# Optimization experiments

Hardware: AMD Instinct MI355X
Metric: run time of the kernel (lower is better)

## Reference

```python
import jax, jax.numpy as jnp
import numpy as np

HIDDEN = 1024
NUM_HEADS = 16
HEAD_DIM = HIDDEN // NUM_HEADS
EPS = 1e-05


def setup_inputs() -> dict:
    key = jax.random.key(0)
    ks = jax.random.split(key, 6)
    B, S = 4, 2048
    x = jax.random.normal(ks[0], (B, S, HIDDEN), dtype=jnp.float32)
    # trunc_normal_(std=0.02) approximated by scaled normal
    w_in = jax.random.normal(ks[1], (3 * HIDDEN, HIDDEN), dtype=jnp.float32) * 0.02
    b_in = jax.random.normal(ks[2], (3 * HIDDEN,), dtype=jnp.float32) * 0.02
    w_norm = jnp.ones((HIDDEN,), dtype=jnp.float32)
    lim = 1.0 / np.sqrt(HIDDEN)
    w_out = jax.random.uniform(ks[3], (HIDDEN, HIDDEN), dtype=jnp.float32, minval=-lim, maxval=lim)
    b_out = jax.random.uniform(ks[4], (HIDDEN,), dtype=jnp.float32, minval=-lim, maxval=lim)
    return {"x": x, "w_in": w_in, "b_in": b_in, "w_norm": w_norm, "w_out": w_out, "b_out": b_out}


def _rms_norm(x, w, eps):
    var = jnp.mean(jnp.square(x), axis=-1, keepdims=True)
    return x * jax.lax.rsqrt(var + eps) * w


def reference(x, w_in, b_in, w_norm, w_out, b_out):
    B, S, _ = x.shape
    xn = _rms_norm(x, w_norm, EPS)
    qkv = jnp.einsum('bsd,ed->bse', xn, w_in) + b_in  # [B,S,3*HIDDEN]
    q, k, v = jnp.split(qkv, 3, axis=-1)
    # [B,S,H*D] -> [B,H,S,D]
    def split_heads(t):
        return t.reshape(B, S, NUM_HEADS, HEAD_DIM).transpose(0, 2, 1, 3)
    q, k, v = split_heads(q), split_heads(k), split_heads(v)
    scale = 1.0 / np.sqrt(HEAD_DIM)
    scores = jnp.einsum('bhqd,bhkd->bhqk', q, k) * scale
    attn = jax.nn.softmax(scores, axis=-1)
    o = jnp.einsum('bhqk,bhkd->bhqd', attn, v)
    o = o.transpose(0, 2, 1, 3).reshape(B, S, HIDDEN)
    return jnp.einsum('bsd,ed->bse', o, w_out) + b_out
```

## Files before the change

### kernel.cpp

```cpp
#include <hip/hip_runtime.h>
#include <stdint.h>

typedef short bf16x4 __attribute__((ext_vector_type(4)));
typedef short bf16x8 __attribute__((ext_vector_type(8)));
typedef _Float16 f16x8 __attribute__((ext_vector_type(8)));
typedef float f32x4 __attribute__((ext_vector_type(4)));
typedef float f32x16 __attribute__((ext_vector_type(16)));
typedef unsigned int u32x4 __attribute__((ext_vector_type(4)));
typedef unsigned int u32x2 __attribute__((ext_vector_type(2)));

#if __has_builtin(__builtin_amdgcn_exp2f)
#define EXP2 __builtin_amdgcn_exp2f
#else
#define EXP2 exp2f
#endif

__device__ __forceinline__ short f2bf(float f) {
  union { float f; uint32_t u; } v; v.f = f;
  uint32_t r = (v.u + 0x7fffu + ((v.u >> 16) & 1u)) >> 16;
  return (short)(uint16_t)r;
}

__device__ __forceinline__ unsigned cvtpk_bf16(float lo, float hi) {
  unsigned r;
  asm("v_cvt_pk_bf16_f32 %0, %1, %2" : "=v"(r) : "v"(lo), "v"(hi));
  return r;
}

#if __has_builtin(__builtin_amdgcn_permlane32_swap)
__device__ __forceinline__ void plane32_swap(unsigned& a, unsigned& b) {
  u32x2 r = __builtin_amdgcn_permlane32_swap(a, b, false, false);
  a = r[0]; b = r[1];
}
__device__ __forceinline__ float xhalf_max(float x) {
  unsigned xu = __builtin_bit_cast(unsigned, x);
  u32x2 r = __builtin_amdgcn_permlane32_swap(xu, xu, false, false);
  return fmaxf(__builtin_bit_cast(float, r[0]), __builtin_bit_cast(float, r[1]));
}
__device__ __forceinline__ float xhalf_sum(float x) {
  unsigned xu = __builtin_bit_cast(unsigned, x);
  u32x2 r = __builtin_amdgcn_permlane32_swap(xu, xu, false, false);
  return __builtin_bit_cast(float, r[0]) + __builtin_bit_cast(float, r[1]);
}
#else
__device__ __forceinline__ void plane32_swap(unsigned& a, unsigned& b) {
  asm("s_nop 1\n\tv_permlane32_swap_b32 %0, %1" : "+v"(a), "+v"(b));
}
__device__ __forceinline__ float xhalf_max(float x) { return fmaxf(x, __shfl_xor(x, 32, 64)); }
__device__ __forceinline__ float xhalf_sum(float x) { return x + __shfl_xor(x, 32, 64); }
#endif

__device__ __forceinline__ float fmax3(float a, float b, float c) {
  return fmaxf(fmaxf(a, b), c);
}

__device__ __forceinline__ float tmax16(const f32x16& s) {
  float a0 = fmax3(s[0], s[1], s[2]);
  float a1 = fmax3(s[3], s[4], s[5]);
  float a2 = fmax3(s[6], s[7], s[8]);
  float a3 = fmax3(s[9], s[10], s[11]);
  float a4 = fmax3(s[12], s[13], s[14]);
  float b0 = fmax3(a0, a1, s[15]);
  float b1 = fmax3(a2, a3, a4);
  return fmaxf(b0, b1);
}
__device__ __forceinline__ float tsum16(const f32x16& s) {
  float a0 = (s[0] + s[1]) + (s[2] + s[3]);
  float a1 = (s[4] + s[5]) + (s[6] + s[7]);
  float a2 = (s[8] + s[9]) + (s[10] + s[11]);
  float a3 = (s[12] + s[13]) + (s[14] + s[15]);
  return (a0 + a1) + (a2 + a3);
}

__device__ __forceinline__ f32x16 zero16() {
  f32x16 z;
#pragma unroll
  for (int i = 0; i < 16; ++i) z[i] = 0.f;
  return z;
}

__device__ __forceinline__ void gld_lds16(const void* g, void* l) {
  __builtin_amdgcn_global_load_lds(
      (__attribute__((address_space(1))) const void*)g,
      (__attribute__((address_space(3))) void*)l, 16, 0, 0);
}

__global__ __launch_bounds__(256) void k_rmsnorm(const float* __restrict__ x,
                                                 const float* __restrict__ wn,
                                                 short* __restrict__ xn) {
  const int row = blockIdx.x;
  const int t = threadIdx.x;
  const float4 v = reinterpret_cast<const float4*>(x + (size_t)row * 1024)[t];
  float ss = v.x * v.x + v.y * v.y + v.z * v.z + v.w * v.w;
#pragma unroll
  for (int m = 32; m >= 1; m >>= 1) ss += __shfl_xor(ss, m, 64);
  __shared__ float red[4];
  if ((t & 63) == 0) red[t >> 6] = ss;
  __syncthreads();
  const float tot = red[0] + red[1] + red[2] + red[3];
  const float rr = rsqrtf(tot * (1.0f / 1024.0f) + 1e-5f);
  const float4 g = reinterpret_cast<const float4*>(wn)[t];
  bf16x4 o;
  o[0] = f2bf(v.x * rr * g.x);
  o[1] = f2bf(v.y * rr * g.y);
  o[2] = f2bf(v.z * rr * g.z);
  o[3] = f2bf(v.w * rr * g.w);
  reinterpret_cast<bf16x4*>(xn + (size_t)row * 1024)[t] = o;
}

__global__ __launch_bounds__(256) void k_cast_bf(const float* __restrict__ in,
                                                 short* __restrict__ out, int n4) {
  int i = blockIdx.x * 256 + threadIdx.x;
  if (i >= n4) return;
  float4 v = reinterpret_cast<const float4*>(in)[i];
  bf16x4 o;
  o[0] = f2bf(v.x); o[1] = f2bf(v.y); o[2] = f2bf(v.z); o[3] = f2bf(v.w);
  reinterpret_cast<bf16x4*>(out)[i] = o;
}

__global__ __launch_bounds__(256) void k_cast_f16(const float* __restrict__ in,
                                                  _Float16* __restrict__ out, int n4) {
  int i = blockIdx.x * 256 + threadIdx.x;
  if (i >= n4) return;
  float4 v = reinterpret_cast<const float4*>(in)[i];
  _Float16 o[4] = {(_Float16)v.x, (_Float16)v.y, (_Float16)v.z, (_Float16)v.w};
  reinterpret_cast<ulong1*>(out)[i] = *reinterpret_cast<ulong1*>(o);
}

__global__ __launch_bounds__(256) void k_gemm_qkv(const short* __restrict__ A,
                                                  const short* __restrict__ B,
                                                  const float* __restrict__ bias,
                                                  short* __restrict__ qb,
                                                  short* __restrict__ kb,
                                                  short* __restrict__ vb) {
  __shared__ __align__(16) short As[128 * 32];
  __shared__ __align__(16) short Bs[128 * 32];
  const int t = threadIdx.x;
  const int orig = blockIdx.y * 24 + blockIdx.x;
  const int swz = (orig & 7) * 192 + (orig >> 3);
  const long bn0 = (long)(swz % 24) * 128;
  const long bm0 = (long)(swz / 24) * 128;
  const int w = t >> 6, l = t & 63;
  const int wr = (w >> 1) * 64, wc = (w & 1) * 64;
  const int lm = l & 15, h = l >> 4;
  f32x4 acc[4][4];
#pragma unroll
  for (int i = 0; i < 4; ++i)
#pragma unroll
    for (int j = 0; j < 4; ++j) acc[i][j] = (f32x4){0.f, 0.f, 0.f, 0.f};
  const int srow = t >> 2, scol = (t & 3) * 8;
  const short* Ag = A + (bm0 + srow) * 1024 + scol;
  const short* Bg = B + (bn0 + srow) * 1024 + scol;
  short* AsP = As + t * 8;
  short* BsP = Bs + t * 8;
  for (int kt = 0; kt < 32; ++kt) {
    const int k0 = kt << 5;
    gld_lds16(Ag + k0, AsP);
    gld_lds16(Ag + k0 + 64 * 1024, AsP + 2048);
    gld_lds16(Bg + k0, BsP);
    gld_lds16(Bg + k0 + 64 * 1024, BsP + 2048);
    __syncthreads();
    bf16x8 af[4], bfr[4];
#pragma unroll
    for (int mi = 0; mi < 4; ++mi)
      af[mi] = *reinterpret_cast<const bf16x8*>(As + (wr + mi * 16 + lm) * 32 + h * 8);
#pragma unroll
    for (int ni = 0; ni < 4; ++ni)
      bfr[ni] = *reinterpret_cast<const bf16x8*>(Bs + (wc + ni * 16 + lm) * 32 + h * 8);
    __builtin_amdgcn_s_setprio(1);
#pragma unroll
    for (int mi = 0; mi < 4; ++mi)
#pragma unroll
      for (int ni = 0; ni < 4; ++ni)
        acc[mi][ni] = __builtin_amdgcn_mfma_f32_16x16x32_bf16(af[mi], bfr[ni], acc[mi][ni], 0, 0, 0);
    __builtin_amdgcn_s_setprio(0);
    __syncthreads();
  }
#pragma unroll
  for (int ni = 0; ni < 4; ++ni) {
    const int ncol = (int)bn0 + wc + ni * 16 + lm;
    const float bv = bias[ncol];
    const int which = ncol >> 10;
    const int e = ncol & 1023;
#pragma unroll
    for (int mi = 0; mi < 4; ++mi) {
#pragma unroll
      for (int r = 0; r < 4; ++r) {
        const long mrow = bm0 + wr + mi * 16 + h * 4 + r;
        const float val = acc[mi][ni][r] + bv;
        const long off = (((mrow >> 11) * 16 + (e >> 6)) * 2048 + (mrow & 2047)) * 64 + (e & 63);
        if (which == 0) qb[off] = f2bf(val * 0.18033688011112042f);
        else if (which == 1) kb[off] = f2bf(val);
        else vb[off] = f2bf(val);
      }
    }
  }
}

__global__ __launch_bounds__(256) void k_gemm_out(const _Float16* __restrict__ A,
                                                  const _Float16* __restrict__ B,
                                                  const float* __restrict__ bias,
                                                  float* __restrict__ outp) {
  __shared__ __align__(16) _Float16 As[128 * 32];
  __shared__ __align__(16) _Float16 Bs[128 * 32];
  const int t = threadIdx.x;
  const int orig = blockIdx.y * 8 + blockIdx.x;
  const int swz = (orig & 7) * 64 + (orig >> 3);
  const long bn0 = (long)(swz % 8) * 128;
  const long bm0 = (long)(swz / 8) * 128;
  const int w = t >> 6, l = t & 63;
  const int wr = (w >> 1) * 64, wc = (w & 1) * 64;
  const int lm = l & 15, h = l >> 4;
  f32x4 acc[4][4];
#pragma unroll
  for (int i = 0; i < 4; ++i)
#pragma unroll
    for (int j = 0; j < 4; ++j) acc[i][j] = (f32x4){0.f, 0.f, 0.f, 0.f};
  const int srow = t >> 2, scol = (t & 3) * 8;
  const _Float16* Ag = A + (bm0 + srow) * 1024 + scol;
  const _Float16* Bg = B + (bn0 + srow) * 1024 + scol;
  _Float16* AsP = As + t * 8;
  _Float16* BsP = Bs + t * 8;
  for (int kt = 0; kt < 32; ++kt) {
    const int k0 = kt << 5;
    gld_lds16(Ag + k0, AsP);
    gld_lds16(Ag + k0 + 64 * 1024, AsP + 2048);
    gld_lds16(Bg + k0, BsP);
    gld_lds16(Bg + k0 + 64 * 1024, BsP + 2048);
    __syncthreads();
    f16x8 af[4], bfr[4];
#pragma unroll
    for (int mi = 0; mi < 4; ++mi)
      af[mi] = *reinterpret_cast<const f16x8*>(As + (wr + mi * 16 + lm) * 32 + h * 8);
#pragma unroll
    for (int ni = 0; ni < 4; ++ni)
      bfr[ni] = *reinterpret_cast<const f16x8*>(Bs + (wc + ni * 16 + lm) * 32 + h * 8);
    __builtin_amdgcn_s_setprio(1);
#pragma unroll
    for (int mi = 0; mi < 4; ++mi)
#pragma unroll
      for (int ni = 0; ni < 4; ++ni)
        acc[mi][ni] = __builtin_amdgcn_mfma_f32_16x16x32_f16(af[mi], bfr[ni], acc[mi][ni], 0, 0, 0);
    __builtin_amdgcn_s_setprio(0);
    __syncthreads();
  }
#pragma unroll
  for (int ni = 0; ni < 4; ++ni) {
    const int ncol = (int)bn0 + wc + ni * 16 + lm;
    const float bv = bias[ncol];
#pragma unroll
    for (int mi = 0; mi < 4; ++mi) {
#pragma unroll
      for (int r = 0; r < 4; ++r) {
        const long mrow = bm0 + wr + mi * 16 + h * 4 + r;
        outp[mrow * 1024 + ncol] = acc[mi][ni][r] + bv;
      }
    }
  }
}

__global__ __launch_bounds__(256) void k_transpose_v(const short* __restrict__ v,
                                                     short* __restrict__ vt) {
  __shared__ short tile[64][72];
  const int bh = blockIdx.y, st = blockIdx.x;
  const int t = threadIdx.x;
  const int r = t >> 2, c0 = (t & 3) * 16;
  const short* src = v + ((size_t)(bh * 2048 + st * 64 + r)) * 64 + c0;
  bf16x8 a = *reinterpret_cast<const bf16x8*>(src);
  bf16x8 b = *reinterpret_cast<const bf16x8*>(src + 8);
#pragma unroll
  for (int j = 0; j < 8; ++j) tile[r][c0 + j] = a[j];
#pragma unroll
  for (int j = 0; j < 8; ++j) tile[r][c0 + 8 + j] = b[j];
  __syncthreads();
  __align__(16) short tmp[16];
#pragma unroll
  for (int j = 0; j < 16; ++j) tmp[j] = tile[c0 + j][r];
  short* dst = vt + ((size_t)(bh * 64 + r)) * 2048 + st * 64 + c0;
  *reinterpret_cast<bf16x8*>(dst) = *reinterpret_cast<const bf16x8*>(tmp);
  *reinterpret_cast<bf16x8*>(dst + 8) = *reinterpret_cast<const bf16x8*>(tmp + 8);
}

__global__ __launch_bounds__(256, 2) void k_attn(const short* __restrict__ q,
                                                 const short* __restrict__ k,
                                                 const short* __restrict__ vt,
                                                 _Float16* __restrict__ o) {
  __shared__ __align__(16) short Ks[4][2048];
  __shared__ __align__(16) short Vs[4][2048];
  const int orig = blockIdx.y * 8 + blockIdx.x;
  const int work = (orig & 7) * 64 + (orig >> 3);
  const int bh = work >> 3;
  const int qt = work & 7;
  const int t = threadIdx.x;
  const int w = t >> 6, l = t & 63;
  const int lq = l & 31, hh = l >> 5;
  const int xr = lq & 7;
  const int qbase = qt * 256 + w * 64;

  bf16x8 qf[2][4];
#pragma unroll
  for (int qh = 0; qh < 2; ++qh) {
    const short* qp = q + ((size_t)(bh * 2048 + qbase + qh * 32 + lq)) * 64 + hh * 8;
#pragma unroll
    for (int db = 0; db < 4; ++db)
      qf[qh][db] = *reinterpret_cast<const bf16x8*>(qp + db * 16);
  }

  const int gg = t;
  const int uK = gg ^ ((gg >> 3) & 7);
  const int vrow = gg >> 2;
  const int vcol = (gg & 3) ^ (vrow & 3);
  const short* kh = k + (size_t)bh * 2048 * 64;
  const short* vh = vt + (size_t)bh * 64 * 2048;
  const short* ksrc = kh + uK * 8;
  const short* vsrc = vh + vrow * 2048 + vcol * 8;

  int koff[4], voff[2][2];
#pragma unroll
  for (int db = 0; db < 4; ++db)
    koff[db] = (lq * 8 + ((db * 2 + hh) ^ xr)) * 8;
#pragma unroll
  for (int dt = 0; dt < 2; ++dt)
#pragma unroll
    for (int kg = 0; kg < 2; ++kg)
      voff[dt][kg] = ((dt * 32 + lq) * 4 + ((kg * 2 + hh) ^ (lq & 3))) * 8;

  f32x16 oa00 = zero16(), oa01 = zero16();
  f32x16 oa10 = zero16(), oa11 = zero16();
  float mr0 = -1e30f, mr1 = -1e30f, lr0 = 0.f, lr1 = 0.f;

#pragma unroll
  for (int p = 0; p < 3; ++p) {
    gld_lds16(ksrc + p * 2048, &Ks[p][gg * 8]);
    gld_lds16(vsrc + p * 32, &Vs[p][gg * 8]);
  }

  for (int kt = 0; kt < 64; ++kt) {
    asm volatile("s_waitcnt vmcnt(4)" ::: "memory");
    __builtin_amdgcn_s_barrier();
    int kn = kt + 3; if (kn > 63) kn = 63;
    gld_lds16(ksrc + kn * 2048, &Ks[(kt + 3) & 3][gg * 8]);
    gld_lds16(vsrc + kn * 32, &Vs[(kt + 3) & 3][gg * 8]);

    const short* kb_ = Ks[kt & 3];
    const short* vb_ = Vs[kt & 3];
    f32x16 s0 = zero16(), s1 = zero16();
    __builtin_amdgcn_s_setprio(1);
#pragma unroll
    for (int db = 0; db < 4; ++db) {
      bf16x8 kf = *reinterpret_cast<const bf16x8*>(kb_ + koff[db]);
      s0 = __builtin_amdgcn_mfma_f32_32x32x16_bf16(kf, qf[0][db], s0, 0, 0, 0);
      s1 = __builtin_amdgcn_mfma_f32_32x32x16_bf16(kf, qf[1][db], s1, 0, 0, 0);
    }
    __builtin_amdgcn_s_setprio(0);
    float tm0 = xhalf_max(tmax16(s0));
    float tm1 = xhalf_max(tmax16(s1));
    if (!__all((tm0 <= mr0 + 8.f) && (tm1 <= mr1 + 8.f))) {
      const float mn0 = fmaxf(mr0, tm0), mn1 = fmaxf(mr1, tm1);
      const float c0 = EXP2(mr0 - mn0), c1 = EXP2(mr1 - mn1);
      lr0 *= c0; lr1 *= c1;
#pragma unroll
      for (int r = 0; r < 16; ++r) {
        oa00[r] *= c0; oa01[r] *= c0;
        oa10[r] *= c1; oa11[r] *= c1;
      }
      mr0 = mn0; mr1 = mn1;
    }
#pragma unroll
    for (int r = 0; r < 16; ++r) {
      s0[r] = EXP2(s0[r] - mr0);
      s1[r] = EXP2(s1[r] - mr1);
    }
    lr0 += tsum16(s0);
    lr1 += tsum16(s1);
    __builtin_amdgcn_s_setprio(1);
#pragma unroll
    for (int kg = 0; kg < 2; ++kg) {
      const int b0 = kg * 8;
      unsigned p00 = cvtpk_bf16(s0[b0 + 0], s0[b0 + 1]);
      unsigned p01 = cvtpk_bf16(s0[b0 + 2], s0[b0 + 3]);
      unsigned p02 = cvtpk_bf16(s0[b0 + 4], s0[b0 + 5]);
      unsigned p03 = cvtpk_bf16(s0[b0 + 6], s0[b0 + 7]);
      plane32_swap(p00, p02);
      plane32_swap(p01, p03);
      u32x4 pw0 = {p00, p01, p02, p03};
      bf16x8 pf0 = *reinterpret_cast<bf16x8*>(&pw0);
      unsigned p10 = cvtpk_bf16(s1[b0 + 0], s1[b0 + 1]);
      unsigned p11 = cvtpk_bf16(s1[b0 + 2], s1[b0 + 3]);
      unsigned p12 = cvtpk_bf16(s1[b0 + 4], s1[b0 + 5]);
      unsigned p13 = cvtpk_bf16(s1[b0 + 6], s1[b0 + 7]);
      plane32_swap(p10, p12);
      plane32_swap(p11, p13);
      u32x4 pw1 = {p10, p11, p12, p13};
      bf16x8 pf1 = *reinterpret_cast<bf16x8*>(&pw1);
      bf16x8 vf0 = *reinterpret_cast<const bf16x8*>(vb_ + voff[0][kg]);
      oa00 = __builtin_amdgcn_mfma_f32_32x32x16_bf16(vf0, pf0, oa00, 0, 0, 0);
      oa10 = __builtin_amdgcn_mfma_f32_32x32x16_bf16(vf0, pf1, oa10, 0, 0, 0);
      bf16x8 vf1 = *reinterpret_cast<const bf16x8*>(vb_ + voff[1][kg]);
      oa01 = __builtin_amdgcn_mfma_f32_32x32x16_bf16(vf1, pf0, oa01, 0, 0, 0);
      oa11 = __builtin_amdgcn_mfma_f32_32x32x16_bf16(vf1, pf1, oa11, 0, 0, 0);
    }
    __builtin_amdgcn_s_setprio(0);
  }
  const float inv0 = 1.0f / xhalf_sum(lr0);
  const float inv1 = 1.0f / xhalf_sum(lr1);
  const int b = bh >> 4, hd = bh & 15;
  _Float16* ob0 = o + ((size_t)(b * 2048 + qbase + lq)) * 1024 + hd * 64;
  _Float16* ob1 = ob0 + 32 * 1024;
#pragma unroll
  for (int r2 = 0; r2 < 16; ++r2) {
    const int d0 = (r2 & 3) + 8 * (r2 >> 2) + 4 * hh;
    ob0[d0] = (_Float16)(oa00[r2] * inv0);
    ob0[d0 + 32] = (_Float16)(oa01[r2] * inv0);
    ob1[d0] = (_Float16)(oa10[r2] * inv1);
    ob1[d0 + 32] = (_Float16)(oa11[r2] * inv1);
  }
}

extern "C" void kernel_launch(void* const* d_in, const int* in_sizes, int n_in,
                              void* d_out, int out_size, void* d_ws, size_t ws_size,
                              hipStream_t stream) {
  const float* x = (const float*)d_in[0];
  const float* w_in = (const float*)d_in[1];
  const float* b_in = (const float*)d_in[2];
  const float* w_norm = (const float*)d_in[3];
  const float* w_out = (const float*)d_in[4];
  const float* b_out = (const float*)d_in[5];
  float* out = (float*)d_out;
  char* ws = (char*)d_ws;
  short* xn = (short*)(ws);
  short* win_b = (short*)(ws + 16777216);
  _Float16* wout_h = (_Float16*)(ws + 23068672);
  short* qb = (short*)(ws + 25165824);
  short* kb = (short*)(ws + 41943040);
  short* vb = (short*)(ws + 58720256);
  short* vt = (short*)(ws + 75497472);
  _Float16* ob = (_Float16*)vb;

  k_cast_bf<<<3072, 256, 0, stream>>>(w_in, win_b, 786432);
  k_cast_f16<<<1024, 256, 0, stream>>>(w_out, wout_h, 262144);
  k_rmsnorm<<<8192, 256, 0, stream>>>(x, w_norm, xn);
  k_gemm_qkv<<<dim3(24, 64), 256, 0, stream>>>(xn, win_b, b_in, qb, kb, vb);
  k_transpose_v<<<dim3(32, 64), 256, 0, stream>>>(vb, vt);
  k_attn<<<dim3(8, 64), 256, 0, stream>>>(qb, kb, vt, ob);
  k_gemm_out<<<dim3(8, 64), 256, 0, stream>>>(ob, wout_h, b_out, out);
}
```

Measured before the change: 227.4 us.

## Give each wave private K/V LDS buffers to remove block barriers

Each of the four waves now loads its own full copy of the K and V tiles into a private LDS region, double-buffered. This removes the per-iteration block-wide barrier. All K/V fragments are read into registers up front, and the next tile's global-to-LDS loads are issued right after those reads complete. The cost is four times the global/L2 traffic for K/V and a larger LDS footprint (64KB per block), plus a prefetch depth cut from 3 stages to 2.

```diff
diff --git a/kernel.cpp b/kernel.cpp
--- a/kernel.cpp
+++ b/kernel.cpp
@@ -285,8 +285,7 @@
                                                  const short* __restrict__ k,
                                                  const short* __restrict__ vt,
                                                  _Float16* __restrict__ o) {
-  __shared__ __align__(16) short Ks[4][2048];
-  __shared__ __align__(16) short Vs[4][2048];
+  __shared__ __align__(16) short lds[4][8192];
   const int orig = blockIdx.y * 8 + blockIdx.x;
   const int work = (orig & 7) * 64 + (orig >> 3);
   const int bh = work >> 3;
@@ -296,6 +295,8 @@
   const int lq = l & 31, hh = l >> 5;
   const int xr = lq & 7;
   const int qbase = qt * 256 + w * 64;
+  short* Kb = &lds[w][0];
+  short* Vb = &lds[w][4096];
 
   bf16x8 qf[2][4];
 #pragma unroll
@@ -306,14 +307,19 @@
       qf[qh][db] = *reinterpret_cast<const bf16x8*>(qp + db * 16);
   }
 
-  const int gg = t;
-  const int uK = gg ^ ((gg >> 3) & 7);
-  const int vrow = gg >> 2;
-  const int vcol = (gg & 3) ^ (vrow & 3);
   const short* kh = k + (size_t)bh * 2048 * 64;
   const short* vh = vt + (size_t)bh * 64 * 2048;
-  const short* ksrc = kh + uK * 8;
-  const short* vsrc = vh + vrow * 2048 + vcol * 8;
+  const short* ks4[4];
+  const short* vs4[4];
+#pragma unroll
+  for (int i = 0; i < 4; ++i) {
+    const int g = i * 64 + l;
+    const int uK = g ^ ((g >> 3) & 7);
+    ks4[i] = kh + uK * 8;
+    const int vr = g >> 2;
+    const int vc = (g & 3) ^ (vr & 3);
+    vs4[i] = vh + vr * 2048 + vc * 8;
+  }
 
   int koff[4], voff[2][2];
 #pragma unroll
@@ -330,27 +336,46 @@
   float mr0 = -1e30f, mr1 = -1e30f, lr0 = 0.f, lr1 = 0.f;
 
 #pragma unroll
-  for (int p = 0; p < 3; ++p) {
-    gld_lds16(ksrc + p * 2048, &Ks[p][gg * 8]);
-    gld_lds16(vsrc + p * 32, &Vs[p][gg * 8]);
-  }
-
+  for (int p = 0; p < 2; ++p) {
+#pragma unroll
+    for (int i = 0; i < 4; ++i)
+      gld_lds16(ks4[i] + p * 2048, Kb + p * 2048 + i * 512 + l * 8);
+#pragma unroll
+    for (int i = 0; i < 4; ++i)
+      gld_lds16(vs4[i] + p * 32, Vb + p * 2048 + i * 512 + l * 8);
+  }
+
+#pragma unroll 2
   for (int kt = 0; kt < 64; ++kt) {
-    asm volatile("s_waitcnt vmcnt(4)" ::: "memory");
-    __builtin_amdgcn_s_barrier();
-    int kn = kt + 3; if (kn > 63) kn = 63;
-    gld_lds16(ksrc + kn * 2048, &Ks[(kt + 3) & 3][gg * 8]);
-    gld_lds16(vsrc + kn * 32, &Vs[(kt + 3) & 3][gg * 8]);
-
-    const short* kb_ = Ks[kt & 3];
-    const short* vb_ = Vs[kt & 3];
+    asm volatile("s_waitcnt vmcnt(8)" ::: "memory");
+    const int buf = kt & 1;
+    const short* kb_ = Kb + buf * 2048;
+    const short* vb_ = Vb + buf * 2048;
+    bf16x8 kf[4], vfr[2][2];
+#pragma unroll
+    for (int db = 0; db < 4; ++db)
+      kf[db] = *reinterpret_cast<const bf16x8*>(kb_ + koff[db]);
+#pragma unroll
+    for (int dt = 0; dt < 2; ++dt)
+#pragma unroll
+      for (int kg = 0; kg < 2; ++kg)
+        vfr[dt][kg] = *reinterpret_cast<const bf16x8*>(vb_ + voff[dt][kg]);
+    asm volatile("s_waitcnt lgkmcnt(0)" ::: "memory");
+    __builtin_amdgcn_sched_barrier(0);
+    int kn = kt + 2; if (kn > 63) kn = 63;
+#pragma unroll
+    for (int i = 0; i < 4; ++i)
+      gld_lds16(ks4[i] + kn * 2048, (short*)kb_ + i * 512 + l * 8);
+#pragma unroll
+    for (int i = 0; i < 4; ++i)
+      gld_lds16(vs4[i] + kn * 32, (short*)vb_ + i * 512 + l * 8);
+
     f32x16 s0 = zero16(), s1 = zero16();
     __builtin_amdgcn_s_setprio(1);
 #pragma unroll
     for (int db = 0; db < 4; ++db) {
-      bf16x8 kf = *reinterpret_cast<const bf16x8*>(kb_ + koff[db]);
-      s0 = __builtin_amdgcn_mfma_f32_32x32x16_bf16(kf, qf[0][db], s0, 0, 0, 0);
-      s1 = __builtin_amdgcn_mfma_f32_32x32x16_bf16(kf, qf[1][db], s1, 0, 0, 0);
+      s0 = __builtin_amdgcn_mfma_f32_32x32x16_bf16(kf[db], qf[0][db], s0, 0, 0, 0);
+      s1 = __builtin_amdgcn_mfma_f32_32x32x16_bf16(kf[db], qf[1][db], s1, 0, 0, 0);
     }
     __builtin_amdgcn_s_setprio(0);
     float tm0 = xhalf_max(tmax16(s0));
@@ -393,12 +418,10 @@
       plane32_swap(p11, p13);
       u32x4 pw1 = {p10, p11, p12, p13};
       bf16x8 pf1 = *reinterpret_cast<bf16x8*>(&pw1);
-      bf16x8 vf0 = *reinterpret_cast<const bf16x8*>(vb_ + voff[0][kg]);
-      oa00 = __builtin_amdgcn_mfma_f32_32x32x16_bf16(vf0, pf0, oa00, 0, 0, 0);
-      oa10 = __builtin_amdgcn_mfma_f32_32x32x16_bf16(vf0, pf1, oa10, 0, 0, 0);
-      bf16x8 vf1 = *reinterpret_cast<const bf16x8*>(vb_ + voff[1][kg]);
-      oa01 = __builtin_amdgcn_mfma_f32_32x32x16_bf16(vf1, pf0, oa01, 0, 0, 0);
-      oa11 = __builtin_amdgcn_mfma_f32_32x32x16_bf16(vf1, pf1, oa11, 0, 0, 0);
+      oa00 = __builtin_amdgcn_mfma_f32_32x32x16_bf16(vfr[0][kg], pf0, oa00, 0, 0, 0);
+      oa10 = __builtin_amdgcn_mfma_f32_32x32x16_bf16(vfr[0][kg], pf1, oa10, 0, 0, 0);
+      oa01 = __builtin_amdgcn_mfma_f32_32x32x16_bf16(vfr[1][kg], pf0, oa01, 0, 0, 0);
+      oa11 = __builtin_amdgcn_mfma_f32_32x32x16_bf16(vfr[1][kg], pf1, oa11, 0, 0, 0);
     }
     __builtin_amdgcn_s_setprio(0);
   }
```

After: 226.6 us. About the same (-0.3%).

## Write K/V in MFMA fragment layout from QKV GEMM, drop V transpose and LDS staging

Applied to the files above, without the earlier changes.

The QKV GEMM epilogue now stores K and V directly in a per-lane MFMA fragment layout, which removes the separate V transpose kernel. The attention kernel then loads K/V fragments straight from global memory into registers with coalesced 16-byte loads, dropping the LDS ring buffer, its barriers and the async global-to-LDS prefetch. The cost is that each wave re-reads K/V from global/L2 instead of sharing them through LDS across 4 waves. It also loses explicit prefetch pipelining and relies on unroll-2 and the compiler to hide latency. The epilogue scatter writes also become more scattered.

```diff
diff --git a/kernel.cpp b/kernel.cpp
--- a/kernel.cpp
+++ b/kernel.cpp
@@ -131,8 +131,8 @@
                                                   const short* __restrict__ B,
                                                   const float* __restrict__ bias,
                                                   short* __restrict__ qb,
-                                                  short* __restrict__ kb,
-                                                  short* __restrict__ vb) {
+                                                  short* __restrict__ kfrag,
+                                                  short* __restrict__ vfrag) {
   __shared__ __align__(16) short As[128 * 32];
   __shared__ __align__(16) short Bs[128 * 32];
   const int t = threadIdx.x;
@@ -182,16 +182,28 @@
     const float bv = bias[ncol];
     const int which = ncol >> 10;
     const int e = ncol & 1023;
+    const int hd = e >> 6, d = e & 63;
 #pragma unroll
     for (int mi = 0; mi < 4; ++mi) {
 #pragma unroll
       for (int r = 0; r < 4; ++r) {
         const long mrow = bm0 + wr + mi * 16 + h * 4 + r;
         const float val = acc[mi][ni][r] + bv;
-        const long off = (((mrow >> 11) * 16 + (e >> 6)) * 2048 + (mrow & 2047)) * 64 + (e & 63);
-        if (which == 0) qb[off] = f2bf(val * 0.18033688011112042f);
-        else if (which == 1) kb[off] = f2bf(val);
-        else vb[off] = f2bf(val);
+        const long bh = (mrow >> 11) * 16 + hd;
+        const int seq = (int)(mrow & 2047);
+        if (which == 0) {
+          const long off = (bh * 2048 + seq) * 64 + d;
+          qb[off] = f2bf(val * 0.18033688011112042f);
+        } else if (which == 1) {
+          const long off = ((bh * 64 + (seq >> 5)) * 4 + (d >> 4)) * 512 +
+                           ((seq & 31) | (((d >> 3) & 1) << 5)) * 8 + (d & 7);
+          kfrag[off] = f2bf(val);
+        } else {
+          const long off = (((bh * 64 + (seq >> 5)) * 2 + (d >> 5)) * 2 +
+                            ((seq >> 4) & 1)) * 512 +
+                           ((d & 31) | (((seq >> 3) & 1) << 5)) * 8 + (seq & 7);
+          vfrag[off] = f2bf(val);
+        }
       }
     }
   }
@@ -259,34 +271,10 @@
   }
 }
 
-__global__ __launch_bounds__(256) void k_transpose_v(const short* __restrict__ v,
-                                                     short* __restrict__ vt) {
-  __shared__ short tile[64][72];
-  const int bh = blockIdx.y, st = blockIdx.x;
-  const int t = threadIdx.x;
-  const int r = t >> 2, c0 = (t & 3) * 16;
-  const short* src = v + ((size_t)(bh * 2048 + st * 64 + r)) * 64 + c0;
-  bf16x8 a = *reinterpret_cast<const bf16x8*>(src);
-  bf16x8 b = *reinterpret_cast<const bf16x8*>(src + 8);
-#pragma unroll
-  for (int j = 0; j < 8; ++j) tile[r][c0 + j] = a[j];
-#pragma unroll
-  for (int j = 0; j < 8; ++j) tile[r][c0 + 8 + j] = b[j];
-  __syncthreads();
-  __align__(16) short tmp[16];
-#pragma unroll
-  for (int j = 0; j < 16; ++j) tmp[j] = tile[c0 + j][r];
-  short* dst = vt + ((size_t)(bh * 64 + r)) * 2048 + st * 64 + c0;
-  *reinterpret_cast<bf16x8*>(dst) = *reinterpret_cast<const bf16x8*>(tmp);
-  *reinterpret_cast<bf16x8*>(dst + 8) = *reinterpret_cast<const bf16x8*>(tmp + 8);
-}
-
-__global__ __launch_bounds__(256, 2) void k_attn(const short* __restrict__ q,
-                                                 const short* __restrict__ k,
-                                                 const short* __restrict__ vt,
-                                                 _Float16* __restrict__ o) {
-  __shared__ __align__(16) short Ks[4][2048];
-  __shared__ __align__(16) short Vs[4][2048];
+__global__ __launch_bounds__(256) void k_attn(const short* __restrict__ q,
+                                              const short* __restrict__ kfrag,
+                                              const short* __restrict__ vfrag,
+                                              _Float16* __restrict__ o) {
   const int orig = blockIdx.y * 8 + blockIdx.x;
   const int work = (orig & 7) * 64 + (orig >> 3);
   const int bh = work >> 3;
@@ -294,7 +282,6 @@
   const int t = threadIdx.x;
   const int w = t >> 6, l = t & 63;
   const int lq = l & 31, hh = l >> 5;
-  const int xr = lq & 7;
   const int qbase = qt * 256 + w * 64;
 
   bf16x8 qf[2][4];
@@ -306,51 +293,33 @@
       qf[qh][db] = *reinterpret_cast<const bf16x8*>(qp + db * 16);
   }
 
-  const int gg = t;
-  const int uK = gg ^ ((gg >> 3) & 7);
-  const int vrow = gg >> 2;
-  const int vcol = (gg & 3) ^ (vrow & 3);
-  const short* kh = k + (size_t)bh * 2048 * 64;
-  const short* vh = vt + (size_t)bh * 64 * 2048;
-  const short* ksrc = kh + uK * 8;
-  const short* vsrc = vh + vrow * 2048 + vcol * 8;
-
-  int koff[4], voff[2][2];
-#pragma unroll
-  for (int db = 0; db < 4; ++db)
-    koff[db] = (lq * 8 + ((db * 2 + hh) ^ xr)) * 8;
-#pragma unroll
-  for (int dt = 0; dt < 2; ++dt)
-#pragma unroll
-    for (int kg = 0; kg < 2; ++kg)
-      voff[dt][kg] = ((dt * 32 + lq) * 4 + ((kg * 2 + hh) ^ (lq & 3))) * 8;
+  const short* kfb = kfrag + (size_t)bh * 64 * 4 * 512 + l * 8;
+  const short* vfb = vfrag + (size_t)bh * 64 * 4 * 512 + l * 8;
 
   f32x16 oa00 = zero16(), oa01 = zero16();
   f32x16 oa10 = zero16(), oa11 = zero16();
   float mr0 = -1e30f, mr1 = -1e30f, lr0 = 0.f, lr1 = 0.f;
 
-#pragma unroll
-  for (int p = 0; p < 3; ++p) {
-    gld_lds16(ksrc + p * 2048, &Ks[p][gg * 8]);
-    gld_lds16(vsrc + p * 32, &Vs[p][gg * 8]);
-  }
-
+#pragma unroll 2
   for (int kt = 0; kt < 64; ++kt) {
-    asm volatile("s_waitcnt vmcnt(4)" ::: "memory");
-    __builtin_amdgcn_s_barrier();
-    int kn = kt + 3; if (kn > 63) kn = 63;
-    gld_lds16(ksrc + kn * 2048, &Ks[(kt + 3) & 3][gg * 8]);
-    gld_lds16(vsrc + kn * 32, &Vs[(kt + 3) & 3][gg * 8]);
-
-    const short* kb_ = Ks[kt & 3];
-    const short* vb_ = Vs[kt & 3];
+    bf16x8 kf[4], vfr[2][2];
+    const short* kp = kfb + (size_t)kt * 4 * 512;
+#pragma unroll
+    for (int db = 0; db < 4; ++db)
+      kf[db] = *reinterpret_cast<const bf16x8*>(kp + db * 512);
+    const short* vp = vfb + (size_t)kt * 4 * 512;
+#pragma unroll
+    for (int dt = 0; dt < 2; ++dt)
+#pragma unroll
+      for (int kg = 0; kg < 2; ++kg)
+        vfr[dt][kg] = *reinterpret_cast<const bf16x8*>(vp + (dt * 2 + kg) * 512);
+
     f32x16 s0 = zero16(), s1 = zero16();
     __builtin_amdgcn_s_setprio(1);
 #pragma unroll
     for (int db = 0; db < 4; ++db) {
-      bf16x8 kf = *reinterpret_cast<const bf16x8*>(kb_ + koff[db]);
-      s0 = __builtin_amdgcn_mfma_f32_32x32x16_bf16(kf, qf[0][db], s0, 0, 0, 0);
-      s1 = __builtin_amdgcn_mfma_f32_32x32x16_bf16(kf, qf[1][db], s1, 0, 0, 0);
+      s0 = __builtin_amdgcn_mfma_f32_32x32x16_bf16(kf[db], qf[0][db], s0, 0, 0, 0);
+      s1 = __builtin_amdgcn_mfma_f32_32x32x16_bf16(kf[db], qf[1][db], s1, 0, 0, 0);
     }
     __builtin_amdgcn_s_setprio(0);
     float tm0 = xhalf_max(tmax16(s0));
@@ -393,12 +362,10 @@
       plane32_swap(p11, p13);
       u32x4 pw1 = {p10, p11, p12, p13};
       bf16x8 pf1 = *reinterpret_cast<bf16x8*>(&pw1);
-      bf16x8 vf0 = *reinterpret_cast<const bf16x8*>(vb_ + voff[0][kg]);
-      oa00 = __builtin_amdgcn_mfma_f32_32x32x16_bf16(vf0, pf0, oa00, 0, 0, 0);
-      oa10 = __builtin_amdgcn_mfma_f32_32x32x16_bf16(vf0, pf1, oa10, 0, 0, 0);
-      bf16x8 vf1 = *reinterpret_cast<const bf16x8*>(vb_ + voff[1][kg]);
-      oa01 = __builtin_amdgcn_mfma_f32_32x32x16_bf16(vf1, pf0, oa01, 0, 0, 0);
-      oa11 = __builtin_amdgcn_mfma_f32_32x32x16_bf16(vf1, pf1, oa11, 0, 0, 0);
+      oa00 = __builtin_amdgcn_mfma_f32_32x32x16_bf16(vfr[0][kg], pf0, oa00, 0, 0, 0);
+      oa10 = __builtin_amdgcn_mfma_f32_32x32x16_bf16(vfr[0][kg], pf1, oa10, 0, 0, 0);
+      oa01 = __builtin_amdgcn_mfma_f32_32x32x16_bf16(vfr[1][kg], pf0, oa01, 0, 0, 0);
+      oa11 = __builtin_amdgcn_mfma_f32_32x32x16_bf16(vfr[1][kg], pf1, oa11, 0, 0, 0);
     }
     __builtin_amdgcn_s_setprio(0);
   }
@@ -432,16 +399,14 @@
   short* win_b = (short*)(ws + 16777216);
   _Float16* wout_h = (_Float16*)(ws + 23068672);
   short* qb = (short*)(ws + 25165824);
-  short* kb = (short*)(ws + 41943040);
-  short* vb = (short*)(ws + 58720256);
-  short* vt = (short*)(ws + 75497472);
-  _Float16* ob = (_Float16*)vb;
+  short* kfrag = (short*)(ws + 41943040);
+  short* vfrag = (short*)(ws + 58720256);
+  _Float16* ob = (_Float16*)(ws + 75497472);
 
   k_cast_bf<<<3072, 256, 0, stream>>>(w_in, win_b, 786432);
   k_cast_f16<<<1024, 256, 0, stream>>>(w_out, wout_h, 262144);
   k_rmsnorm<<<8192, 256, 0, stream>>>(x, w_norm, xn);
-  k_gemm_qkv<<<dim3(24, 64), 256, 0, stream>>>(xn, win_b, b_in, qb, kb, vb);
-  k_transpose_v<<<dim3(32, 64), 256, 0, stream>>>(vb, vt);
-  k_attn<<<dim3(8, 64), 256, 0, stream>>>(qb, kb, vt, ob);
+  k_gemm_qkv<<<dim3(24, 64), 256, 0, stream>>>(xn, win_b, b_in, qb, kfrag, vfrag);
+  k_attn<<<dim3(8, 64), 256, 0, stream>>>(qb, kfrag, vfrag, ob);
   k_gemm_out<<<dim3(8, 64), 256, 0, stream>>>(ob, wout_h, b_out, out);
 }
```

Measured after the change: 255.1 us. 1.12x slower.
